# Performance work log

Measured on AMD Instinct MI355X. Metric: run time of the kernel, lower is better.

## Reference

```python
import jax, jax.numpy as jnp
import numpy as np

N_NODES = 100000
FEAT = 256
HID = 128
REL = 2
BATCH = 20000
K = 10  # filtersize


def setup_inputs() -> dict:
    key = jax.random.key(0)
    k1, k2, k3, k4, k5 = jax.random.split(key, 5)
    nodes = jax.random.randint(k1, (BATCH,), 0, N_NODES)
    neigh_idx = jax.random.randint(k2, (REL, BATCH, K), 0, N_NODES)
    features = jax.random.normal(k3, (N_NODES, FEAT), dtype=jnp.float32)
    W_stc = jax.random.normal(k4, (REL, FEAT, HID), dtype=jnp.float32) * (1.0 / np.sqrt(FEAT))
    W_det = jax.random.normal(k5, (FEAT + REL * HID, HID), dtype=jnp.float32) * (1.0 / np.sqrt(FEAT + REL * HID))
    return {"nodes": nodes, "neigh_idx": neigh_idx, "features": features,
            "W_stc": W_stc, "W_det": W_det}


def reference(nodes, neigh_idx, features, W_stc, W_det):
    # self features: irregular gather [B, F]
    self_feats = features[nodes]
    # per-relation neighbor gather [R, B, K, F] -> mean over sampled neighbors [R, B, F]
    neigh_mean = features[neigh_idx].mean(axis=2)
    # STC layer projection to hidden per relation: [R, B, H]
    neigh_h = jnp.einsum('rbf,rfh->rbh', neigh_mean, W_stc)
    # concat self feats with each relation's neighbor embedding: [B, F + R*H]
    combined = jnp.concatenate(
        [self_feats, jnp.moveaxis(neigh_h, 0, 1).reshape(neigh_h.shape[1], -1)], axis=1)
    # linear + relu (dropout_flag=False -> no dropout)
    return jax.nn.relu(combined @ W_det)
```

## Files before the change

kernel.cpp:

```cpp
#include <hip/hip_runtime.h>
#include <hip/hip_bf16.h>

#define N_NODES 100000
#define FEAT    256
#define HID     128
#define REL     2
#define BATCH   20000
#define KNEI    10

typedef short bf16x8 __attribute__((ext_vector_type(8)));
typedef float f32x4  __attribute__((ext_vector_type(4)));

__device__ __forceinline__ unsigned short f2bf(float x) {
    union { float f; unsigned u; } v; v.f = x;
    unsigned r = v.u + 0x7fffu + ((v.u >> 16) & 1u);
    return (unsigned short)(r >> 16);
}

__global__ __launch_bounds__(256) void prep_B(const float* __restrict__ W_stc,
                                              const float* __restrict__ W_det,
                                              unsigned short* __restrict__ Bsw) {
    int tid = blockIdx.x * 256 + threadIdx.x;
    int j    = tid & 7;
    int lane = (tid >> 3) & 63;
    int nt   = (tid >> 9) & 7;
    int kt   = tid >> 12;
    int k = kt * 32 + ((lane >> 4) * 8) + j;
    int n = nt * 16 + (lane & 15);

    float val;
    if (k < 256) {
        val = W_det[k * HID + n];
    } else {
        int rel = (k >= 512) ? 1 : 0;
        int f = k - 256 - rel * 256;
        const float* ws = W_stc + (rel * FEAT + f) * HID;
        const float* wd = W_det + (256 + rel * HID) * HID + n;
        float s = 0.f;
        #pragma unroll 8
        for (int j2 = 0; j2 < HID; ++j2) s += ws[j2] * wd[j2 * HID];
        val = s;
    }
    Bsw[tid] = f2bf(val);
}

__global__ __launch_bounds__(64) void gather_mean(const int* __restrict__ nodes,
                                                  const int* __restrict__ neigh_idx,
                                                  const float* __restrict__ features,
                                                  unsigned short* __restrict__ A) {
    const int b = blockIdx.x;
    const int t = threadIdx.x;
    const float4* F4 = (const float4*)features;

    const int self = nodes[b];
    float4 sf = F4[(size_t)self * 64 + t];

    float4 s0 = make_float4(0.f, 0.f, 0.f, 0.f);
    float4 s1 = make_float4(0.f, 0.f, 0.f, 0.f);
    const int* idx0 = neigh_idx + (size_t)0 * BATCH * KNEI + (size_t)b * KNEI;
    const int* idx1 = neigh_idx + (size_t)1 * BATCH * KNEI + (size_t)b * KNEI;
    #pragma unroll
    for (int k = 0; k < KNEI; ++k) {
        float4 v = F4[(size_t)idx0[k] * 64 + t];
        s0.x += v.x; s0.y += v.y; s0.z += v.z; s0.w += v.w;
    }
    #pragma unroll
    for (int k = 0; k < KNEI; ++k) {
        float4 v = F4[(size_t)idx1[k] * 64 + t];
        s1.x += v.x; s1.y += v.y; s1.z += v.z; s1.w += v.w;
    }
    const float inv = 1.0f / (float)KNEI;

    ushort4* Arow = (ushort4*)(A + (size_t)b * 768);
    ushort4 p;
    p.x = f2bf(sf.x); p.y = f2bf(sf.y); p.z = f2bf(sf.z); p.w = f2bf(sf.w);
    Arow[t] = p;
    p.x = f2bf(s0.x * inv); p.y = f2bf(s0.y * inv); p.z = f2bf(s0.z * inv); p.w = f2bf(s0.w * inv);
    Arow[64 + t] = p;
    p.x = f2bf(s1.x * inv); p.y = f2bf(s1.y * inv); p.z = f2bf(s1.z * inv); p.w = f2bf(s1.w * inv);
    Arow[128 + t] = p;
}

__global__ __launch_bounds__(256) void gemm_relu(const unsigned short* __restrict__ A,
                                                 const unsigned short* __restrict__ Bsw,
                                                 float* __restrict__ out) {
    const int wave = (blockIdx.x * 256 + threadIdx.x) >> 6;
    if (wave >= BATCH / 16) return;
    const int lane = threadIdx.x & 63;
    const int quad = lane >> 4;
    const int l16  = lane & 15;

    const unsigned short* arow = A + ((size_t)(wave * 16 + l16)) * 768 + quad * 8;

    f32x4 acc[8];
    #pragma unroll
    for (int nt = 0; nt < 8; ++nt) acc[nt] = (f32x4){0.f, 0.f, 0.f, 0.f};

    #pragma unroll 4
    for (int kt = 0; kt < 24; ++kt) {
        bf16x8 a = *(const bf16x8*)(arow + kt * 32);
        const unsigned short* bk = Bsw + ((size_t)(kt * 8) * 64 + lane) * 8;
        #pragma unroll
        for (int nt = 0; nt < 8; ++nt) {
            bf16x8 bfr = *(const bf16x8*)(bk + (size_t)nt * 64 * 8);
            acc[nt] = __builtin_amdgcn_mfma_f32_16x16x32_bf16(a, bfr, acc[nt], 0, 0, 0);
        }
    }

    float* orow = out + (size_t)(wave * 16) * HID;
    #pragma unroll
    for (int nt = 0; nt < 8; ++nt) {
        #pragma unroll
        for (int r = 0; r < 4; ++r) {
            int row = quad * 4 + r;
            int col = nt * 16 + l16;
            float v = acc[nt][r];
            orow[(size_t)row * HID + col] = v > 0.f ? v : 0.f;
        }
    }
}

extern "C" void kernel_launch(void* const* d_in, const int* in_sizes, int n_in,
                              void* d_out, int out_size, void* d_ws, size_t ws_size,
                              hipStream_t stream) {
    const int*   nodes     = (const int*)d_in[0];
    const int*   neigh_idx = (const int*)d_in[1];
    const float* features  = (const float*)d_in[2];
    const float* W_stc     = (const float*)d_in[3];
    const float* W_det     = (const float*)d_in[4];
    float* out = (float*)d_out;

    unsigned short* Bsw = (unsigned short*)d_ws;
    unsigned short* A   = (unsigned short*)((char*)d_ws + 256 * 1024);

    prep_B<<<(768 * 128) / 256, 256, 0, stream>>>(W_stc, W_det, Bsw);
    gather_mean<<<BATCH, 64, 0, stream>>>(nodes, neigh_idx, features, A);
    gemm_relu<<<(BATCH / 16 + 3) / 4, 256, 0, stream>>>(A, Bsw, out);
}
```

Measured before the change: 231.9 us.

## Fuse neighbor gather-mean with MFMA GEMM via shared-memory A tile

```diff
diff --git a/kernel.cpp b/kernel.cpp
--- a/kernel.cpp
+++ b/kernel.cpp
@@ -8,6 +8,9 @@
 #define BATCH   20000
 #define KNEI    10
 
+#define APAD    8
+#define AROW    (768 + APAD)
+
 typedef short bf16x8 __attribute__((ext_vector_type(8)));
 typedef float f32x4  __attribute__((ext_vector_type(4)));
 
@@ -17,106 +20,116 @@
     return (unsigned short)(r >> 16);
 }
 
+__device__ __forceinline__ ushort4 pack4(float a, float b, float c, float d) {
+    ushort4 p; p.x = f2bf(a); p.y = f2bf(b); p.z = f2bf(c); p.w = f2bf(d);
+    return p;
+}
+
+__device__ __forceinline__ size_t bsw_index(int k, int n) {
+    int kt = k >> 5, j = k & 7, hi = (k >> 3) & 3;
+    int lane = hi * 16 + (n & 15), nt = n >> 4;
+    return ((size_t)(kt * 8 + nt) * 64 + lane) * 8 + j;
+}
+
 __global__ __launch_bounds__(256) void prep_B(const float* __restrict__ W_stc,
                                               const float* __restrict__ W_det,
                                               unsigned short* __restrict__ Bsw) {
-    int tid = blockIdx.x * 256 + threadIdx.x;
-    int j    = tid & 7;
-    int lane = (tid >> 3) & 63;
-    int nt   = (tid >> 9) & 7;
-    int kt   = tid >> 12;
-    int k = kt * 32 + ((lane >> 4) * 8) + j;
-    int n = nt * 16 + (lane & 15);
-
-    float val;
-    if (k < 256) {
-        val = W_det[k * HID + n];
+    const int blk = blockIdx.x;
+    const int tid = threadIdx.x;
+    if (blk < 32) {
+        const int rel   = blk >> 4;
+        const int fbase = (blk & 15) * 16;
+        const int n     = tid & 127;
+        const int fh    = tid >> 7;
+        const float* wd = W_det + (size_t)(256 + rel * HID) * HID + n;
+        #pragma unroll
+        for (int fo = 0; fo < 8; ++fo) {
+            const int f = fbase + fh * 8 + fo;
+            const float* ws = W_stc + (size_t)(rel * FEAT + f) * HID;
+            float acc = 0.f;
+            #pragma unroll 8
+            for (int j2 = 0; j2 < HID; ++j2) acc += ws[j2] * wd[(size_t)j2 * HID];
+            const int k = 256 + rel * 256 + f;
+            Bsw[bsw_index(k, n)] = f2bf(acc);
+        }
     } else {
-        int rel = (k >= 512) ? 1 : 0;
-        int f = k - 256 - rel * 256;
-        const float* ws = W_stc + (rel * FEAT + f) * HID;
-        const float* wd = W_det + (256 + rel * HID) * HID + n;
-        float s = 0.f;
-        #pragma unroll 8
-        for (int j2 = 0; j2 < HID; ++j2) s += ws[j2] * wd[j2 * HID];
-        val = s;
+        const int base = (blk - 32) * 16384;
+        #pragma unroll 4
+        for (int i = 0; i < 64; ++i) {
+            const int idx = base + i * 256 + tid;
+            const int k = idx >> 7, n = idx & 127;
+            Bsw[bsw_index(k, n)] = f2bf(W_det[idx]);
+        }
     }
-    Bsw[tid] = f2bf(val);
 }
 
-__global__ __launch_bounds__(64) void gather_mean(const int* __restrict__ nodes,
-                                                  const int* __restrict__ neigh_idx,
-                                                  const float* __restrict__ features,
-                                                  unsigned short* __restrict__ A) {
-    const int b = blockIdx.x;
-    const int t = threadIdx.x;
+__global__ __launch_bounds__(256, 4) void fused(const int* __restrict__ nodes,
+                                                const int* __restrict__ neigh_idx,
+                                                const float* __restrict__ features,
+                                                const unsigned short* __restrict__ Bsw,
+                                                float* __restrict__ out) {
+    __shared__ unsigned short As[16 * AROW];
+
+    const int blk  = blockIdx.x;
+    const int w    = threadIdx.x >> 6;
+    const int lane = threadIdx.x & 63;
     const float4* F4 = (const float4*)features;
-
-    const int self = nodes[b];
-    float4 sf = F4[(size_t)self * 64 + t];
-
-    float4 s0 = make_float4(0.f, 0.f, 0.f, 0.f);
-    float4 s1 = make_float4(0.f, 0.f, 0.f, 0.f);
-    const int* idx0 = neigh_idx + (size_t)0 * BATCH * KNEI + (size_t)b * KNEI;
-    const int* idx1 = neigh_idx + (size_t)1 * BATCH * KNEI + (size_t)b * KNEI;
-    #pragma unroll
-    for (int k = 0; k < KNEI; ++k) {
-        float4 v = F4[(size_t)idx0[k] * 64 + t];
-        s0.x += v.x; s0.y += v.y; s0.z += v.z; s0.w += v.w;
-    }
-    #pragma unroll
-    for (int k = 0; k < KNEI; ++k) {
-        float4 v = F4[(size_t)idx1[k] * 64 + t];
-        s1.x += v.x; s1.y += v.y; s1.z += v.z; s1.w += v.w;
-    }
     const float inv = 1.0f / (float)KNEI;
 
-    ushort4* Arow = (ushort4*)(A + (size_t)b * 768);
-    ushort4 p;
-    p.x = f2bf(sf.x); p.y = f2bf(sf.y); p.z = f2bf(sf.z); p.w = f2bf(sf.w);
-    Arow[t] = p;
-    p.x = f2bf(s0.x * inv); p.y = f2bf(s0.y * inv); p.z = f2bf(s0.z * inv); p.w = f2bf(s0.w * inv);
-    Arow[64 + t] = p;
-    p.x = f2bf(s1.x * inv); p.y = f2bf(s1.y * inv); p.z = f2bf(s1.z * inv); p.w = f2bf(s1.w * inv);
-    Arow[128 + t] = p;
-}
+    #pragma unroll
+    for (int e = 0; e < 4; ++e) {
+        const int m = w * 4 + e;
+        const int b = blk * 16 + m;
+        const int self = nodes[b];
+        const int* i0 = neigh_idx + (size_t)b * KNEI;
+        const int* i1 = neigh_idx + (size_t)(BATCH + b) * KNEI;
 
-__global__ __launch_bounds__(256) void gemm_relu(const unsigned short* __restrict__ A,
-                                                 const unsigned short* __restrict__ Bsw,
-                                                 float* __restrict__ out) {
-    const int wave = (blockIdx.x * 256 + threadIdx.x) >> 6;
-    if (wave >= BATCH / 16) return;
-    const int lane = threadIdx.x & 63;
+        float4 sf = F4[(size_t)self * 64 + lane];
+        float4 s0 = make_float4(0.f, 0.f, 0.f, 0.f);
+        float4 s1 = make_float4(0.f, 0.f, 0.f, 0.f);
+        #pragma unroll
+        for (int k = 0; k < KNEI; ++k) {
+            float4 v = F4[(size_t)i0[k] * 64 + lane];
+            s0.x += v.x; s0.y += v.y; s0.z += v.z; s0.w += v.w;
+        }
+        #pragma unroll
+        for (int k = 0; k < KNEI; ++k) {
+            float4 v = F4[(size_t)i1[k] * 64 + lane];
+            s1.x += v.x; s1.y += v.y; s1.z += v.z; s1.w += v.w;
+        }
+        ushort4* row = (ushort4*)(As + m * AROW);
+        row[lane]       = pack4(sf.x, sf.y, sf.z, sf.w);
+        row[64 + lane]  = pack4(s0.x * inv, s0.y * inv, s0.z * inv, s0.w * inv);
+        row[128 + lane] = pack4(s1.x * inv, s1.y * inv, s1.z * inv, s1.w * inv);
+    }
+    __syncthreads();
+
     const int quad = lane >> 4;
     const int l16  = lane & 15;
+    const unsigned short* a_base = As + l16 * AROW + quad * 8;
 
-    const unsigned short* arow = A + ((size_t)(wave * 16 + l16)) * 768 + quad * 8;
+    f32x4 acc0 = (f32x4){0.f, 0.f, 0.f, 0.f};
+    f32x4 acc1 = (f32x4){0.f, 0.f, 0.f, 0.f};
+    const int nt0 = w, nt1 = w + 4;
 
-    f32x4 acc[8];
     #pragma unroll
-    for (int nt = 0; nt < 8; ++nt) acc[nt] = (f32x4){0.f, 0.f, 0.f, 0.f};
-
-    #pragma unroll 4
     for (int kt = 0; kt < 24; ++kt) {
-        bf16x8 a = *(const bf16x8*)(arow + kt * 32);
+        bf16x8 a = *(const bf16x8*)(a_base + kt * 32);
         const unsigned short* bk = Bsw + ((size_t)(kt * 8) * 64 + lane) * 8;
-        #pragma unroll
-        for (int nt = 0; nt < 8; ++nt) {
-            bf16x8 bfr = *(const bf16x8*)(bk + (size_t)nt * 64 * 8);
-            acc[nt] = __builtin_amdgcn_mfma_f32_16x16x32_bf16(a, bfr, acc[nt], 0, 0, 0);
-        }
+        bf16x8 b0 = *(const bf16x8*)(bk + (size_t)nt0 * 64 * 8);
+        bf16x8 b1 = *(const bf16x8*)(bk + (size_t)nt1 * 64 * 8);
+        acc0 = __builtin_amdgcn_mfma_f32_16x16x32_bf16(a, b0, acc0, 0, 0, 0);
+        acc1 = __builtin_amdgcn_mfma_f32_16x16x32_bf16(a, b1, acc1, 0, 0, 0);
     }
 
-    float* orow = out + (size_t)(wave * 16) * HID;
+    float* orow = out + (size_t)(blk * 16) * HID;
     #pragma unroll
-    for (int nt = 0; nt < 8; ++nt) {
-        #pragma unroll
-        for (int r = 0; r < 4; ++r) {
-            int row = quad * 4 + r;
-            int col = nt * 16 + l16;
-            float v = acc[nt][r];
-            orow[(size_t)row * HID + col] = v > 0.f ? v : 0.f;
-        }
+    for (int r = 0; r < 4; ++r) {
+        const int row = quad * 4 + r;
+        float v0 = acc0[r];
+        float v1 = acc1[r];
+        orow[(size_t)row * HID + nt0 * 16 + l16] = v0 > 0.f ? v0 : 0.f;
+        orow[(size_t)row * HID + nt1 * 16 + l16] = v1 > 0.f ? v1 : 0.f;
     }
 }
 
@@ -131,9 +144,7 @@
     float* out = (float*)d_out;
 
     unsigned short* Bsw = (unsigned short*)d_ws;
-    unsigned short* A   = (unsigned short*)((char*)d_ws + 256 * 1024);
 
-    prep_B<<<(768 * 128) / 256, 256, 0, stream>>>(W_stc, W_det, Bsw);
-    gather_mean<<<BATCH, 64, 0, stream>>>(nodes, neigh_idx, features, A);
-    gemm_relu<<<(BATCH / 16 + 3) / 4, 256, 0, stream>>>(A, Bsw, out);
+    prep_B<<<34, 256, 0, stream>>>(W_stc, W_det, Bsw);
+    fused<<<BATCH / 16, 256, 0, stream>>>(nodes, neigh_idx, features, Bsw, out);
 }
```

Measured after the change: 231.6 us. Within noise of the previous version (-0.1%).
